# Performance work log

Hardware: AMD Instinct MI355X
Metric: run time of the kernel (lower is better)

## Reference

```python
import jax, jax.numpy as jnp
import numpy as np

N_CELLS = 19683   # 27**3 lattice
K = 26            # Moore-neighborhood max_neighbors
D = 128           # state_size
HG = 64           # gating hidden
CNF_STEPS = 3     # integration_steps
DT = 0.1


def setup_inputs() -> dict:
    key = jax.random.key(0)
    ks = jax.random.split(key, 12)
    s = lambda fan_in: 1.0 / np.sqrt(fan_in)
    return {
        "current_state": jax.random.normal(ks[0], (N_CELLS, D), jnp.float32),
        "neighbor_states": jax.random.normal(ks[1], (N_CELLS, K, D), jnp.float32),
        "conn_type": jax.random.randint(ks[2], (N_CELLS, K), 0, 3, jnp.int32),
        "W_local": jax.random.normal(ks[3], (2 * D, D), jnp.float32) * s(2 * D),
        "b_local": jnp.zeros((D,), jnp.float32),
        "W_msg": jax.random.normal(ks[4], (2 * D, D), jnp.float32) * s(2 * D),
        "b_msg": jnp.zeros((D,), jnp.float32),
        "W_upd": jax.random.normal(ks[5], (2 * D, D), jnp.float32) * s(2 * D),
        "b_upd": jnp.zeros((D,), jnp.float32),
        "W_cnf": jax.random.normal(ks[6], (2 * D, D), jnp.float32) * s(2 * D),
        "b_cnf": jnp.zeros((D,), jnp.float32),
        "W_g1": jax.random.normal(ks[7], (D, HG), jnp.float32) * s(D),
        "b_g1": jnp.zeros((HG,), jnp.float32),
        "W_g2": jax.random.normal(ks[8], (HG, 3), jnp.float32) * s(HG),
        "b_g2": jnp.zeros((3,), jnp.float32),
    }


def _masked_mean(nbr, mask):
    # nbr: [N,K,D], mask: [N,K] float -> [N,D]
    cnt = jnp.maximum(mask.sum(-1, keepdims=True), 1.0)
    return jnp.einsum("nkd,nk->nd", nbr, mask) / cnt


def reference(current_state, neighbor_states, conn_type,
              W_local, b_local, W_msg, b_msg, W_upd, b_upd,
              W_cnf, b_cnf, W_g1, b_g1, W_g2, b_g2):
    cur = current_state                       # [N,D]
    nbr = neighbor_states                     # [N,K,D]
    m_l = (conn_type == 0).astype(cur.dtype)  # local mask   [N,K]
    m_f = (conn_type == 1).astype(cur.dtype)  # functional
    m_d = (conn_type == 2).astype(cur.dtype)  # distant

    # --- local expert: SimpleLinear over [cell, mean(local neighbors)] ---
    agg_l = _masked_mean(nbr, m_l)
    local_out = jnp.tanh(jnp.concatenate([cur, agg_l], -1) @ W_local + b_local)

    # --- functional expert: GNN message passing ---
    cur_b = jnp.broadcast_to(cur[:, None, :], nbr.shape)          # [N,K,D]
    edge_in = jnp.concatenate([cur_b, nbr], -1)                   # [N,K,2D]
    msgs = jax.nn.relu(edge_in @ W_msg + b_msg)                   # [N,K,D]
    agg_msg = _masked_mean(msgs, m_f)                             # [N,D]
    func_out = jnp.tanh(jnp.concatenate([cur, agg_msg], -1) @ W_upd + b_upd)

    # --- distant expert: lightweight CNF (fixed-step Euler) ---
    agg_d = _masked_mean(nbr, m_d)

    def euler_step(s, _):
        ds = jnp.tanh(jnp.concatenate([s, agg_d], -1) @ W_cnf + b_cnf)
        return s + DT * ds, None

    distant_out, _ = jax.lax.scan(euler_step, cur, None, length=CNF_STEPS)

    # --- gating network: softmax over 3 experts ---
    gates = jax.nn.softmax(jax.nn.relu(cur @ W_g1 + b_g1) @ W_g2 + b_g2, -1)  # [N,3]

    out = (gates[:, 0:1] * local_out
           + gates[:, 1:2] * func_out
           + gates[:, 2:3] * distant_out)
    return out
```

## Files before the change

### kernel.cpp

```cpp
#include <hip/hip_runtime.h>
#include <math.h>

#define NC 19683
#define KN 26
#define DD 128
#define HGN 64
#define LDSB 136
#define DTC 0.1f
#define CPW 8
#define CPB 32
#define SLOTB 13312

using bf8v = __attribute__((ext_vector_type(8))) short;
using f4v  = __attribute__((ext_vector_type(4))) float;

typedef __attribute__((address_space(1))) const void g_void;
typedef __attribute__((address_space(3))) void l_void;

#define WAITV(N) asm volatile("s_waitcnt vmcnt(" #N ")" ::: "memory")

static __device__ __forceinline__ unsigned short f2bf(float x) {
    union { float f; unsigned u; } v; v.f = x;
    unsigned r = v.u + 0x7fffu + ((v.u >> 16) & 1u);
    return (unsigned short)(r >> 16);
}
static __device__ __forceinline__ unsigned pk2(float a, float b) {
    return ((unsigned)f2bf(a)) | (((unsigned)f2bf(b)) << 16);
}
static __device__ __forceinline__ bf8v cvt8(float4 lo, float4 hi) {
    union { bf8v v; unsigned d[4]; } u;
    asm volatile("v_cvt_pk_bf16_f32 %0, %1, %2" : "=v"(u.d[0]) : "v"(lo.x), "v"(lo.y));
    asm volatile("v_cvt_pk_bf16_f32 %0, %1, %2" : "=v"(u.d[1]) : "v"(lo.z), "v"(lo.w));
    asm volatile("v_cvt_pk_bf16_f32 %0, %1, %2" : "=v"(u.d[2]) : "v"(hi.x), "v"(hi.y));
    asm volatile("v_cvt_pk_bf16_f32 %0, %1, %2" : "=v"(u.d[3]) : "v"(hi.z), "v"(hi.w));
    return u.v;
}

__global__ __launch_bounds__(256) void k_prep(const float* __restrict__ Wl,
    const float* __restrict__ Wm, const float* __restrict__ Wu,
    const float* __restrict__ Wc, const float* __restrict__ Wg1,
    unsigned short* __restrict__ WT, unsigned short* __restrict__ WgT)
{
    int idx = blockIdx.x * 256 + threadIdx.x;
    if (idx < 131072) {
        int m = idx >> 15;
        int r = idx & 32767;
        int j = r >> 8;
        int i = r & 255;
        const float* src = (m == 0) ? Wl : (m == 1) ? Wm : (m == 2) ? Wu : Wc;
        WT[idx] = f2bf(src[i * DD + j]);
    } else {
        int idx2 = idx - 131072;
        int col = idx2 >> 7;
        int k = idx2 & 127;
        WgT[idx2] = f2bf(Wg1[k * HGN + col]);
    }
}

__global__ __launch_bounds__(256, 1) void kE(const float* __restrict__ cur,
    const float* __restrict__ nbr, const int* __restrict__ conn,
    const unsigned short* __restrict__ WT, const float* __restrict__ b_msg,
    unsigned short* __restrict__ agg_l, unsigned short* __restrict__ agg_m,
    unsigned short* __restrict__ agg_d)
{
    __shared__ __align__(16) char LDSA[157696];
    float* Pb = (float*)(LDSA + 106496);
    unsigned short* Wt = (unsigned short*)(LDSA + 122880);

    int t = threadIdx.x;
    int n0 = blockIdx.x * CPB;
    int w = t >> 6, lane = t & 63;
    int lm = lane & 15, lq = lane >> 4;
    int cw0 = n0 + w * CPW;

    int ctv[CPW];
    #pragma unroll
    for (int i = 0; i < CPW; ++i) {
        int n = cw0 + i;
        ctv[i] = (n < NC && lane < KN) ? conn[(size_t)n * KN + lane] : 3;
    }

    {
        const unsigned short* Wm2 = WT + 32768 + 128;
        for (int p = 0; p < 8; ++p) {
            int ch = p * 256 + t;
            int j = ch >> 4, i8 = (ch & 15) * 8;
            *(bf8v*)&Wt[j * LDSB + i8] = *(const bf8v*)&Wm2[j * 256 + i8];
        }
    }

    {
        const unsigned short* Wm1 = WT + 32768;
        bf8v afrP[2][4];
        #pragma unroll
        for (int mt2 = 0; mt2 < 2; ++mt2) {
            int gr = n0 + mt2 * 16 + lm;
            if (gr >= NC) gr = NC - 1;
            const float* rb = &cur[(size_t)gr * DD];
            #pragma unroll
            for (int s = 0; s < 4; ++s) {
                float4 lo = *(const float4*)&rb[s * 32 + lq * 8];
                float4 hi = *(const float4*)&rb[s * 32 + lq * 8 + 4];
                afrP[mt2][s] = cvt8(lo, hi);
            }
        }
        for (int nt = 0; nt < 2; ++nt) {
            int col0 = w * 32 + nt * 16;
            float bm = b_msg[col0 + lm];
            const unsigned short* bb = &Wm1[(col0 + lm) * 256 + lq * 8];
            for (int mt2 = 0; mt2 < 2; ++mt2) {
                f4v acc = {0.f, 0.f, 0.f, 0.f};
                #pragma unroll
                for (int s = 0; s < 4; ++s) {
                    bf8v b = *(const bf8v*)&bb[s * 32];
                    acc = __builtin_amdgcn_mfma_f32_16x16x32_bf16(afrP[mt2][s], b, acc, 0, 0, 0);
                }
                for (int r = 0; r < 4; ++r) {
                    int row = mt2 * 16 + lq * 4 + r;
                    Pb[row * DD + col0 + lm] = acc[r] + bm;
                }
            }
        }
    }
    __syncthreads();

    int rlo = lane >> 5;
    unsigned wb = (unsigned)(lane & 31) * 16;
    auto stage = [&](int i) {
        int nn = cw0 + i; if (nn >= NC) nn = NC - 1;
        const char* cellbase = (const char*)(nbr + (size_t)nn * KN * DD);
        char* slot = LDSA + (size_t)(w * 2 + (i & 1)) * SLOTB;
        #pragma unroll
        for (int j = 0; j < 13; ++j) {
            int row = 2 * j + rlo;
            const char* src = cellbase + (size_t)row * 512 + (wb ^ ((unsigned)(row & 7) << 4));
            __builtin_amdgcn_global_load_lds((g_void*)src, (l_void*)(slot + j * 1024), 16, 0, 0);
        }
    };

    stage(0);
    for (int i = 0; i < CPW; ++i) {
        int n = cw0 + i;
        if (n >= NC) break;
        if (i + 1 < CPW) stage(i + 1);
        if (i == 0) WAITV(13);
        else if (i + 1 < CPW) WAITV(23);
        else WAITV(10);
        __builtin_amdgcn_sched_barrier(0);

        const char* slot = LDSA + (size_t)(w * 2 + (i & 1)) * SLOTB;
        int ct = ctv[i];
        unsigned long long mlb = __ballot(ct == 0);
        unsigned long long mfb = __ballot(ct == 1);
        unsigned long long mdb = __ballot(ct == 2);
        float icl = 1.f / fmaxf((float)__builtin_popcountll(mlb), 1.f);
        float icf = 1.f / fmaxf((float)__builtin_popcountll(mfb), 1.f);
        float icd = 1.f / fmaxf((float)__builtin_popcountll(mdb), 1.f);

        float slx = 0.f, sly = 0.f, sdx = 0.f, sdy = 0.f;
        #pragma unroll
        for (int k = 0; k < KN; ++k) {
            float2 v = *(const float2*)(slot + (size_t)k * 512 + (((unsigned)lane * 8) ^ ((unsigned)(k & 7) << 4)));
            if ((mlb >> k) & 1) { slx += v.x; sly += v.y; }
            if ((mdb >> k) & 1) { sdx += v.x; sdy += v.y; }
        }
        *(unsigned*)&agg_l[(size_t)n * DD + lane * 2] = pk2(slx * icl, sly * icl);
        *(unsigned*)&agg_d[(size_t)n * DD + lane * 2] = pk2(sdx * icd, sdy * icd);

        bf8v afr[2][4];
        #pragma unroll
        for (int mt2 = 0; mt2 < 2; ++mt2) {
            int row = mt2 * 16 + lm;
            unsigned X = (unsigned)(row & 7) << 4;
            const char* rb = slot + (size_t)row * 512;
            #pragma unroll
            for (int s = 0; s < 4; ++s) {
                unsigned b0 = (unsigned)(s * 128 + lq * 32);
                float4 lo = *(const float4*)(rb + (b0 ^ X));
                float4 hi = *(const float4*)(rb + ((b0 + 16) ^ X));
                afr[mt2][s] = cvt8(lo, hi);
            }
        }

        int prow = (w * CPW + i) * DD;
        #pragma unroll
        for (int nt = 0; nt < 8; ++nt) {
            float pv = Pb[prow + nt * 16 + lm];
            f4v a0 = {0.f, 0.f, 0.f, 0.f}, a1 = {0.f, 0.f, 0.f, 0.f};
            #pragma unroll
            for (int s = 0; s < 4; ++s) {
                bf8v b = *(const bf8v*)&Wt[(nt * 16 + lm) * LDSB + s * 32 + lq * 8];
                a0 = __builtin_amdgcn_mfma_f32_16x16x32_bf16(afr[0][s], b, a0, 0, 0, 0);
                a1 = __builtin_amdgcn_mfma_f32_16x16x32_bf16(afr[1][s], b, a1, 0, 0, 0);
            }
            float msum = 0.f;
            #pragma unroll
            for (int r = 0; r < 4; ++r) {
                int rr = lq * 4 + r;
                if ((mfb >> rr) & 1) msum += fmaxf(pv + a0[r], 0.f);
                int rr2 = 16 + lq * 4 + r;
                if ((mfb >> rr2) & 1) msum += fmaxf(pv + a1[r], 0.f);
            }
            msum += __shfl_xor(msum, 16, 64);
            msum += __shfl_xor(msum, 32, 64);
            if (lane < 16) agg_m[(size_t)n * DD + nt * 16 + lane] = f2bf(msum * icf);
        }
    }
}

__global__ __launch_bounds__(256) void kC(const float* __restrict__ cur,
    const unsigned short* __restrict__ WT, const unsigned short* __restrict__ WgT,
    const unsigned short* __restrict__ agg_l, const unsigned short* __restrict__ agg_m,
    const unsigned short* __restrict__ agg_d,
    const float* __restrict__ b_local, const float* __restrict__ b_upd,
    const float* __restrict__ b_cnf, const float* __restrict__ bg1,
    const float* __restrict__ Wg2, const float* __restrict__ bg2,
    float* __restrict__ out)
{
    __shared__ __align__(16) unsigned short Wl[128][LDSB];
    __shared__ __align__(16) unsigned short Xc[32][LDSB];
    __shared__ __align__(16) unsigned short Xa[32][LDSB];
    __shared__ float hrelu[32][HGN + 4];
    __shared__ float glds[32][4];
    __shared__ float bl[DD], bu[DD], bc[DD];
    __shared__ float Wg2s[HGN * 3];
    __shared__ float bg2s[4];
    int t = threadIdx.x;
    int n0 = blockIdx.x * 32;
    int w = t >> 6, lane = t & 63;
    int mt = w & 1, colh = w >> 1;
    int lm = lane & 15, lq = lane >> 4;

    auto stageW = [&](int m, int koff) {
        const unsigned short* src = WT + m * 32768 + koff;
        for (int p = 0; p < 8; ++p) {
            int ch = p * 256 + t;
            int j = ch >> 4, i8 = (ch & 15) * 8;
            *(bf8v*)&Wl[j][i8] = *(const bf8v*)&src[j * 256 + i8];
        }
    };
    auto stageXa = [&](const unsigned short* src) {
        for (int p = 0; p < 2; ++p) {
            int idx = p * 256 + t;
            int r = idx >> 4, c8 = (idx & 15) * 8;
            bf8v v = {0, 0, 0, 0, 0, 0, 0, 0};
            if (n0 + r < NC) v = *(const bf8v*)&src[(size_t)(n0 + r) * DD + c8];
            *(bf8v*)&Xa[r][c8] = v;
        }
    };
    auto mfmaPass = [&](unsigned short (&X)[32][LDSB], f4v* acc) {
        for (int nt = 0; nt < 4; ++nt) {
            int col0 = colh * 64 + nt * 16;
            for (int s = 0; s < 4; ++s) {
                bf8v a = *(const bf8v*)&X[mt * 16 + lm][s * 32 + lq * 8];
                bf8v b = *(const bf8v*)&Wl[col0 + lm][s * 32 + lq * 8];
                acc[nt] = __builtin_amdgcn_mfma_f32_16x16x32_bf16(a, b, acc[nt], 0, 0, 0);
            }
        }
    };

    for (int p = 0; p < 8; ++p) {
        int idx = p * 256 + t;
        int r = idx >> 6, c2 = (idx & 63) * 2;
        float2 v = {0.f, 0.f};
        if (n0 + r < NC) v = *(const float2*)&cur[(size_t)(n0 + r) * DD + c2];
        *(unsigned*)&Xc[r][c2] = pk2(v.x, v.y);
    }
    for (int p = 0; p < 4; ++p) {
        int ch = p * 256 + t;
        int j = ch >> 4, i8 = (ch & 15) * 8;
        *(bf8v*)&Wl[j][i8] = *(const bf8v*)&WgT[j * 128 + i8];
    }
    if (t < 128) { bl[t] = b_local[t]; bu[t] = b_upd[t]; bc[t] = b_cnf[t]; }
    for (int i = t; i < HGN * 3; i += 256) Wg2s[i] = Wg2[i];
    if (t < 3) bg2s[t] = bg2[t];
    __syncthreads();

    {
        int col0 = w * 16;
        float bg = bg1[col0 + lm];
        for (int mt2 = 0; mt2 < 2; ++mt2) {
            f4v acc = {0.f, 0.f, 0.f, 0.f};
            for (int s = 0; s < 4; ++s) {
                bf8v a = *(const bf8v*)&Xc[mt2 * 16 + lm][s * 32 + lq * 8];
                bf8v b = *(const bf8v*)&Wl[col0 + lm][s * 32 + lq * 8];
                acc = __builtin_amdgcn_mfma_f32_16x16x32_bf16(a, b, acc, 0, 0, 0);
            }
            for (int r = 0; r < 4; ++r)
                hrelu[mt2 * 16 + lq * 4 + r][col0 + lm] = fmaxf(acc[r] + bg, 0.f);
        }
    }
    __syncthreads();

    stageW(0, 0);
    if (t < 96) {
        int r = t / 3, e = t - r * 3;
        float s = bg2s[e];
        for (int g = 0; g < HGN; ++g) s += hrelu[r][g] * Wg2s[g * 3 + e];
        glds[r][e] = s;
    }
    __syncthreads();

    if (t < 32) {
        float l0 = glds[t][0], l1 = glds[t][1], l2 = glds[t][2];
        float m = fmaxf(l0, fmaxf(l1, l2));
        float e0 = expf(l0 - m), e1 = expf(l1 - m), e2 = expf(l2 - m);
        float inv = 1.f / (e0 + e1 + e2);
        glds[t][0] = e0 * inv; glds[t][1] = e1 * inv; glds[t][2] = e2 * inv;
    }
    f4v oacc[4], acc[4];
    for (int nt = 0; nt < 4; ++nt) oacc[nt] = (f4v){0.f, 0.f, 0.f, 0.f};

    for (int nt = 0; nt < 4; ++nt) acc[nt] = (f4v){0.f, 0.f, 0.f, 0.f};
    mfmaPass(Xc, acc);
    __syncthreads();
    stageW(0, 128); stageXa(agg_l);
    __syncthreads();
    mfmaPass(Xa, acc);
    for (int nt = 0; nt < 4; ++nt) {
        int col = colh * 64 + nt * 16 + lm;
        for (int r = 0; r < 4; ++r) {
            int row = mt * 16 + lq * 4 + r;
            oacc[nt][r] += glds[row][0] * tanhf(acc[nt][r] + bl[col]);
        }
    }

    __syncthreads();
    stageW(2, 0);
    __syncthreads();
    for (int nt = 0; nt < 4; ++nt) acc[nt] = (f4v){0.f, 0.f, 0.f, 0.f};
    mfmaPass(Xc, acc);
    __syncthreads();
    stageW(2, 128); stageXa(agg_m);
    __syncthreads();
    mfmaPass(Xa, acc);
    for (int nt = 0; nt < 4; ++nt) {
        int col = colh * 64 + nt * 16 + lm;
        for (int r = 0; r < 4; ++r) {
            int row = mt * 16 + lq * 4 + r;
            oacc[nt][r] += glds[row][1] * tanhf(acc[nt][r] + bu[col]);
        }
    }

    __syncthreads();
    stageW(3, 128); stageXa(agg_d);
    __syncthreads();
    for (int nt = 0; nt < 4; ++nt) acc[nt] = (f4v){0.f, 0.f, 0.f, 0.f};
    mfmaPass(Xa, acc);
    f4v hd[4], s[4];
    for (int nt = 0; nt < 4; ++nt) {
        int col = colh * 64 + nt * 16 + lm;
        for (int r = 0; r < 4; ++r) {
            int row = mt * 16 + lq * 4 + r;
            int n = n0 + row;
            hd[nt][r] = acc[nt][r] + bc[col];
            s[nt][r] = (n < NC) ? cur[(size_t)n * DD + col] : 0.f;
        }
    }
    __syncthreads();
    stageW(3, 0);
    for (int step = 0; step < 3; ++step) {
        for (int nt = 0; nt < 4; ++nt) {
            int col = colh * 64 + nt * 16 + lm;
            for (int r = 0; r < 4; ++r) {
                int row = mt * 16 + lq * 4 + r;
                Xa[row][col] = f2bf(s[nt][r]);
            }
        }
        __syncthreads();
        for (int nt = 0; nt < 4; ++nt) acc[nt] = (f4v){0.f, 0.f, 0.f, 0.f};
        mfmaPass(Xa, acc);
        for (int nt = 0; nt < 4; ++nt)
            for (int r = 0; r < 4; ++r)
                s[nt][r] += DTC * tanhf(acc[nt][r] + hd[nt][r]);
        __syncthreads();
    }

    for (int nt = 0; nt < 4; ++nt) {
        int col = colh * 64 + nt * 16 + lm;
        for (int r = 0; r < 4; ++r) {
            int row = mt * 16 + lq * 4 + r;
            int n = n0 + row;
            if (n < NC) out[(size_t)n * DD + col] = oacc[nt][r] + glds[row][2] * s[nt][r];
        }
    }
}

extern "C" void kernel_launch(void* const* d_in, const int* in_sizes, int n_in,
                              void* d_out, int out_size, void* d_ws, size_t ws_size,
                              hipStream_t stream) {
    const float* cur     = (const float*)d_in[0];
    const float* nbr     = (const float*)d_in[1];
    const int*   conn    = (const int*)d_in[2];
    const float* W_local = (const float*)d_in[3];
    const float* b_local = (const float*)d_in[4];
    const float* W_msg   = (const float*)d_in[5];
    const float* b_msg   = (const float*)d_in[6];
    const float* W_upd   = (const float*)d_in[7];
    const float* b_upd   = (const float*)d_in[8];
    const float* W_cnf   = (const float*)d_in[9];
    const float* b_cnf   = (const float*)d_in[10];
    const float* Wg1     = (const float*)d_in[11];
    const float* bg1     = (const float*)d_in[12];
    const float* Wg2     = (const float*)d_in[13];
    const float* bg2     = (const float*)d_in[14];
    float* out = (float*)d_out;

    char* ws = (char*)d_ws;
    unsigned short* WT   = (unsigned short*)ws;
    unsigned short* WgT  = (unsigned short*)(ws + 262144);
    unsigned short* aggl = (unsigned short*)(ws + 278528);
    unsigned short* aggm = aggl + (size_t)NC * DD;
    unsigned short* aggd = aggm + (size_t)NC * DD;

    hipLaunchKernelGGL(k_prep, dim3(544), dim3(256), 0, stream,
                       W_local, W_msg, W_upd, W_cnf, Wg1, WT, WgT);
    hipLaunchKernelGGL(kE, dim3((NC + CPB - 1) / CPB), dim3(256), 0, stream,
                       cur, nbr, conn, WT, b_msg, aggl, aggm, aggd);
    hipLaunchKernelGGL(kC, dim3(616), dim3(256), 0, stream, cur, WT, WgT, aggl, aggm, aggd,
                       b_local, b_upd, b_cnf, bg1, Wg2, bg2, out);
}
```

Baseline: 492.2 us.

## Share neighbor staging across block waves and shrink LDS for two blocks per CU

```diff
diff --git a/kernel.cpp b/kernel.cpp
--- a/kernel.cpp
+++ b/kernel.cpp
@@ -7,9 +7,7 @@
 #define HGN 64
 #define LDSB 136
 #define DTC 0.1f
-#define CPW 8
-#define CPB 32
-#define SLOTB 13312
+#define CPB 40
 
 using bf8v = __attribute__((ext_vector_type(8))) short;
 using f4v  = __attribute__((ext_vector_type(4))) float;
@@ -18,6 +16,7 @@
 typedef __attribute__((address_space(3))) void l_void;
 
 #define WAITV(N) asm volatile("s_waitcnt vmcnt(" #N ")" ::: "memory")
+#define WAITL()  asm volatile("s_waitcnt lgkmcnt(0)" ::: "memory")
 
 static __device__ __forceinline__ unsigned short f2bf(float x) {
     union { float f; unsigned u; } v; v.f = x;
@@ -26,6 +25,9 @@
 }
 static __device__ __forceinline__ unsigned pk2(float a, float b) {
     return ((unsigned)f2bf(a)) | (((unsigned)f2bf(b)) << 16);
+}
+static __device__ __forceinline__ float bf2f(unsigned short u) {
+    union { float f; unsigned v; } w; w.v = ((unsigned)u) << 16; return w.f;
 }
 static __device__ __forceinline__ bf8v cvt8(float4 lo, float4 hi) {
     union { bf8v v; unsigned d[4]; } u;
@@ -57,28 +59,24 @@
     }
 }
 
-__global__ __launch_bounds__(256, 1) void kE(const float* __restrict__ cur,
+__global__ __launch_bounds__(256, 2) void kE(const float* __restrict__ cur,
     const float* __restrict__ nbr, const int* __restrict__ conn,
     const unsigned short* __restrict__ WT, const float* __restrict__ b_msg,
     unsigned short* __restrict__ agg_l, unsigned short* __restrict__ agg_m,
     unsigned short* __restrict__ agg_d)
 {
-    __shared__ __align__(16) char LDSA[157696];
-    float* Pb = (float*)(LDSA + 106496);
-    unsigned short* Wt = (unsigned short*)(LDSA + 122880);
+    __shared__ __align__(16) char LDSA[77888];
+    unsigned short* Wt   = (unsigned short*)LDSA;
+    unsigned short* Pb   = (unsigned short*)(LDSA + 61440);
+    int*            connL = (int*)(LDSA + 73728);
 
     int t = threadIdx.x;
     int n0 = blockIdx.x * CPB;
+    int ng = NC - n0; if (ng > CPB) ng = CPB;
     int w = t >> 6, lane = t & 63;
     int lm = lane & 15, lq = lane >> 4;
-    int cw0 = n0 + w * CPW;
-
-    int ctv[CPW];
-    #pragma unroll
-    for (int i = 0; i < CPW; ++i) {
-        int n = cw0 + i;
-        ctv[i] = (n < NC && lane < KN) ? conn[(size_t)n * KN + lane] : 3;
-    }
+    int rlo = lane >> 5;
+    unsigned wb = (unsigned)(lane & 31) * 16;
 
     {
         const unsigned short* Wm2 = WT + 32768 + 128;
@@ -88,84 +86,82 @@
             *(bf8v*)&Wt[j * LDSB + i8] = *(const bf8v*)&Wm2[j * 256 + i8];
         }
     }
-
+    for (int idx = t; idx < ng * KN; idx += 256)
+        connL[idx] = conn[(size_t)n0 * KN + idx];
     {
         const unsigned short* Wm1 = WT + 32768;
-        bf8v afrP[2][4];
-        #pragma unroll
-        for (int mt2 = 0; mt2 < 2; ++mt2) {
-            int gr = n0 + mt2 * 16 + lm;
-            if (gr >= NC) gr = NC - 1;
+        for (int rt = 0; rt < 3; ++rt) {
+            int gr = n0 + rt * 16 + lm; if (gr >= NC) gr = NC - 1;
             const float* rb = &cur[(size_t)gr * DD];
+            bf8v afrP[4];
             #pragma unroll
             for (int s = 0; s < 4; ++s) {
                 float4 lo = *(const float4*)&rb[s * 32 + lq * 8];
                 float4 hi = *(const float4*)&rb[s * 32 + lq * 8 + 4];
-                afrP[mt2][s] = cvt8(lo, hi);
-            }
-        }
-        for (int nt = 0; nt < 2; ++nt) {
-            int col0 = w * 32 + nt * 16;
-            float bm = b_msg[col0 + lm];
-            const unsigned short* bb = &Wm1[(col0 + lm) * 256 + lq * 8];
-            for (int mt2 = 0; mt2 < 2; ++mt2) {
+                afrP[s] = cvt8(lo, hi);
+            }
+            for (int ntp = 0; ntp < 2; ++ntp) {
+                int col0 = w * 32 + ntp * 16;
+                float bm = b_msg[col0 + lm];
+                const unsigned short* bb = &Wm1[(col0 + lm) * 256 + lq * 8];
                 f4v acc = {0.f, 0.f, 0.f, 0.f};
                 #pragma unroll
                 for (int s = 0; s < 4; ++s) {
                     bf8v b = *(const bf8v*)&bb[s * 32];
-                    acc = __builtin_amdgcn_mfma_f32_16x16x32_bf16(afrP[mt2][s], b, acc, 0, 0, 0);
+                    acc = __builtin_amdgcn_mfma_f32_16x16x32_bf16(afrP[s], b, acc, 0, 0, 0);
                 }
                 for (int r = 0; r < 4; ++r) {
-                    int row = mt2 * 16 + lq * 4 + r;
-                    Pb[row * DD + col0 + lm] = acc[r] + bm;
+                    int row = rt * 16 + lq * 4 + r;
+                    Pb[row * DD + col0 + lm] = f2bf(acc[r] + bm);
                 }
             }
         }
     }
     __syncthreads();
 
-    int rlo = lane >> 5;
-    unsigned wb = (unsigned)(lane & 31) * 16;
     auto stage = [&](int i) {
-        int nn = cw0 + i; if (nn >= NC) nn = NC - 1;
-        const char* cellbase = (const char*)(nbr + (size_t)nn * KN * DD);
-        char* slot = LDSA + (size_t)(w * 2 + (i & 1)) * SLOTB;
-        #pragma unroll
-        for (int j = 0; j < 13; ++j) {
+        const char* cb = (const char*)(nbr + (size_t)(n0 + i) * KN * DD);
+        char* slot = LDSA + 34816 + ((i & 1) ? 13312 : 0);
+        for (int j = w; j < 13; j += 4) {
             int row = 2 * j + rlo;
-            const char* src = cellbase + (size_t)row * 512 + (wb ^ ((unsigned)(row & 7) << 4));
+            const char* src = cb + (size_t)row * 512 + (wb ^ ((unsigned)(row & 7) << 4));
             __builtin_amdgcn_global_load_lds((g_void*)src, (l_void*)(slot + j * 1024), 16, 0, 0);
         }
     };
 
     stage(0);
-    for (int i = 0; i < CPW; ++i) {
-        int n = cw0 + i;
-        if (n >= NC) break;
-        if (i + 1 < CPW) stage(i + 1);
-        if (i == 0) WAITV(13);
-        else if (i + 1 < CPW) WAITV(23);
-        else WAITV(10);
+    for (int g = 0; g < ng; ++g) {
+        if (g + 1 < ng) {
+            stage(g + 1);
+            if (w == 0) { WAITV(4); } else { WAITV(3); }
+        } else {
+            WAITV(0);
+        }
         __builtin_amdgcn_sched_barrier(0);
-
-        const char* slot = LDSA + (size_t)(w * 2 + (i & 1)) * SLOTB;
-        int ct = ctv[i];
+        __builtin_amdgcn_s_barrier();
+
+        const char* slot = LDSA + 34816 + ((g & 1) ? 13312 : 0);
+        size_t n = n0 + g;
+        int ct = (lane < KN) ? connL[g * KN + lane] : 3;
         unsigned long long mlb = __ballot(ct == 0);
         unsigned long long mfb = __ballot(ct == 1);
         unsigned long long mdb = __ballot(ct == 2);
-        float icl = 1.f / fmaxf((float)__builtin_popcountll(mlb), 1.f);
         float icf = 1.f / fmaxf((float)__builtin_popcountll(mfb), 1.f);
-        float icd = 1.f / fmaxf((float)__builtin_popcountll(mdb), 1.f);
-
-        float slx = 0.f, sly = 0.f, sdx = 0.f, sdy = 0.f;
-        #pragma unroll
-        for (int k = 0; k < KN; ++k) {
-            float2 v = *(const float2*)(slot + (size_t)k * 512 + (((unsigned)lane * 8) ^ ((unsigned)(k & 7) << 4)));
-            if ((mlb >> k) & 1) { slx += v.x; sly += v.y; }
-            if ((mdb >> k) & 1) { sdx += v.x; sdy += v.y; }
-        }
-        *(unsigned*)&agg_l[(size_t)n * DD + lane * 2] = pk2(slx * icl, sly * icl);
-        *(unsigned*)&agg_d[(size_t)n * DD + lane * 2] = pk2(sdx * icd, sdy * icd);
+
+        if (w == (g & 3)) {
+            float icl = 1.f / fmaxf((float)__builtin_popcountll(mlb), 1.f);
+            float icd = 1.f / fmaxf((float)__builtin_popcountll(mdb), 1.f);
+            float slx = 0.f, sly = 0.f, sdx = 0.f, sdy = 0.f;
+            #pragma unroll
+            for (int k = 0; k < KN; ++k) {
+                float2 v = *(const float2*)(slot + (size_t)k * 512 +
+                           (((unsigned)lane * 8) ^ ((unsigned)(k & 7) << 4)));
+                if ((mlb >> k) & 1) { slx += v.x; sly += v.y; }
+                if ((mdb >> k) & 1) { sdx += v.x; sdy += v.y; }
+            }
+            *(unsigned*)&agg_l[n * DD + lane * 2] = pk2(slx * icl, sly * icl);
+            *(unsigned*)&agg_d[n * DD + lane * 2] = pk2(sdx * icd, sdy * icd);
+        }
 
         bf8v afr[2][4];
         #pragma unroll
@@ -182,10 +178,10 @@
             }
         }
 
-        int prow = (w * CPW + i) * DD;
         #pragma unroll
-        for (int nt = 0; nt < 8; ++nt) {
-            float pv = Pb[prow + nt * 16 + lm];
+        for (int ntp = 0; ntp < 2; ++ntp) {
+            int nt = w * 2 + ntp;
+            float pv = bf2f(Pb[g * DD + nt * 16 + lm]);
             f4v a0 = {0.f, 0.f, 0.f, 0.f}, a1 = {0.f, 0.f, 0.f, 0.f};
             #pragma unroll
             for (int s = 0; s < 4; ++s) {
@@ -203,8 +199,11 @@
             }
             msum += __shfl_xor(msum, 16, 64);
             msum += __shfl_xor(msum, 32, 64);
-            if (lane < 16) agg_m[(size_t)n * DD + nt * 16 + lane] = f2bf(msum * icf);
-        }
+            if (lane < 16) agg_m[n * DD + nt * 16 + lane] = f2bf(msum * icf);
+        }
+
+        WAITL();
+        __builtin_amdgcn_s_barrier();
     }
 }
 
```

Measured after the change: 475.0 us. 3.5% less time.
